# Optimization experiments

Measured on AMD Instinct MI355X. Metric: run time of the kernel, lower is better.

## Reference

```python
import jax, jax.numpy as jnp
import numpy as np

N_LIST = [2048, 2048]
N_CUM = np.cumsum([0] + N_LIST)


def _chamfer(xo, yo):
    # xo: [B, M, 3], yo: [B, N, 3]
    diff = xo[:, :, None, :] - yo[:, None, :, :]        # [B, M, N, 3]
    dist = jnp.sqrt(jnp.sum(diff * diff, axis=-1))       # [B, M, N]
    mean_x = jnp.mean(jnp.min(dist, axis=2))             # x -> nearest y
    mean_y = jnp.mean(jnp.min(dist, axis=1))             # y -> nearest x
    return mean_x + mean_y


def setup_inputs() -> dict:
    key = jax.random.key(0)
    kx, ky = jax.random.split(key)
    x = jax.random.normal(kx, (8, 4096, 3), dtype=jnp.float32)
    y = jax.random.normal(ky, (8, 4096, 3), dtype=jnp.float32)
    return {"x": x, "y": y}


def reference(x, y):
    # loss_type='chamfer', probability=1 -> top-k over ALL distances == plain mean.
    loss = jnp.float32(0.0)
    for i in range(len(N_LIST)):
        lo, hi = int(N_CUM[i]), int(N_CUM[i + 1])
        loss = loss + _chamfer(x[:, lo:hi], y[:, lo:hi])
    return loss
```

## Files before the change

### kernel.cpp

```cpp
#include <hip/hip_runtime.h>
#include <math.h>

typedef float v2f __attribute__((ext_vector_type(2)));

#if __has_builtin(__builtin_elementwise_fma)
#define FMA2(a, b, c) __builtin_elementwise_fma((a), (b), (c))
#else
static __device__ __forceinline__ v2f FMA2(v2f a, v2f b, v2f c) {
    v2f r; r.x = fmaf(a.x, b.x, c.x); r.y = fmaf(a.y, b.y, c.y); return r;
}
#endif

#define NBATCH 8
#define PTOT   4096
#define NG     2048
#define S      16
#define SLEN   (NG / S)
#define QPT    8
#define NT     256
#define NPROB  32
#define NBLK1  (NPROB * S)
#define NPART  (NPROB * S * NG)

__global__ __launch_bounds__(256) void chamfer_pass1(
    const float* __restrict__ x, const float* __restrict__ y,
    float* __restrict__ pmin)
{
    __shared__ float  raw[SLEN * 3];
    __shared__ float4 refX[SLEN / 4];
    __shared__ float4 refY[SLEN / 4];
    __shared__ float4 refZ[SLEN / 4];
    __shared__ float4 refW[SLEN / 4];

    const int blk   = blockIdx.x;
    const int tid   = threadIdx.x;
    const int slice = blk & (S - 1);
    const int prob  = blk >> 4;
    const int dir   = prob >> 4;
    const int bg    = prob & 15;
    const int b     = bg >> 1;
    const int g     = bg & 1;

    const float* qb = (dir == 0 ? x : y) + (size_t)(b * PTOT + g * NG) * 3;
    const float* rb = (dir == 0 ? y : x) + (size_t)(b * PTOT + g * NG) * 3;

    if (tid < (SLEN * 3) / 4) {
        float4 v = ((const float4*)(rb + slice * SLEN * 3))[tid];
        ((float4*)raw)[tid] = v;
    }

    float4 qv[6];
    {
        const float4* qp = (const float4*)(qb + (size_t)tid * QPT * 3);
        #pragma unroll
        for (int i = 0; i < 6; i++) qv[i] = qp[i];
    }

    __syncthreads();

    if (tid < SLEN / 4) {
        const float* p = raw + tid * 12;
        float x0 = p[0], y0 = p[1],  z0 = p[2];
        float x1 = p[3], y1 = p[4],  z1 = p[5];
        float x2 = p[6], y2 = p[7],  z2 = p[8];
        float x3 = p[9], y3 = p[10], z3 = p[11];
        refX[tid] = make_float4(x0, x1, x2, x3);
        refY[tid] = make_float4(y0, y1, y2, y3);
        refZ[tid] = make_float4(z0, z1, z2, z3);
        refW[tid] = make_float4(fmaf(x0, x0, fmaf(y0, y0, z0 * z0)),
                                fmaf(x1, x1, fmaf(y1, y1, z1 * z1)),
                                fmaf(x2, x2, fmaf(y2, y2, z2 * z2)),
                                fmaf(x3, x3, fmaf(y3, y3, z3 * z3)));
    }

    v2f ax2[QPT], ay2[QPT], az2[QPT];
    float qn[QPT], mn[QPT];
    const float* qf = reinterpret_cast<const float*>(qv);
    #pragma unroll
    for (int k = 0; k < QPT; k++) {
        float qx = qf[k * 3 + 0];
        float qy = qf[k * 3 + 1];
        float qz = qf[k * 3 + 2];
        float ax = -2.0f * qx, ay = -2.0f * qy, az = -2.0f * qz;
        ax2[k] = (v2f){ax, ax};
        ay2[k] = (v2f){ay, ay};
        az2[k] = (v2f){az, az};
        qn[k] = fmaf(qx, qx, fmaf(qy, qy, qz * qz));
        mn[k] = 3.4e38f;
    }

    __syncthreads();

    #pragma unroll 2
    for (int n4 = 0; n4 < SLEN / 4; n4++) {
        float4 X = refX[n4], Y = refY[n4], Z = refZ[n4], W = refW[n4];
        v2f X01 = (v2f){X.x, X.y}, X23 = (v2f){X.z, X.w};
        v2f Y01 = (v2f){Y.x, Y.y}, Y23 = (v2f){Y.z, Y.w};
        v2f Z01 = (v2f){Z.x, Z.y}, Z23 = (v2f){Z.z, Z.w};
        v2f W01 = (v2f){W.x, W.y}, W23 = (v2f){W.z, W.w};
        #pragma unroll
        for (int k = 0; k < QPT; k++) {
            v2f t01 = FMA2(X01, ax2[k], W01);
            t01     = FMA2(Y01, ay2[k], t01);
            t01     = FMA2(Z01, az2[k], t01);
            v2f t23 = FMA2(X23, ax2[k], W23);
            t23     = FMA2(Y23, ay2[k], t23);
            t23     = FMA2(Z23, az2[k], t23);
            mn[k] = fminf(fminf(t01.x, t01.y), mn[k]);
            mn[k] = fminf(fminf(t23.x, t23.y), mn[k]);
        }
    }

    float* op = pmin + (size_t)(prob * S + slice) * NG + tid * QPT;
    #pragma unroll
    for (int k = 0; k < QPT; k++)
        op[k] = mn[k] + qn[k];
}

__global__ __launch_bounds__(256) void chamfer_pass2(
    const float* __restrict__ pmin, float* __restrict__ bsum)
{
    __shared__ float s4[4];
    const int gid  = blockIdx.x * 256 + threadIdx.x;
    const int prob = gid >> 11;
    const int q    = gid & (NG - 1);

    float m0 = 3.4e38f, m1 = 3.4e38f;
    #pragma unroll
    for (int s = 0; s < S; s += 2) {
        m0 = fminf(m0, pmin[(size_t)(prob * S + s) * NG + q]);
        m1 = fminf(m1, pmin[(size_t)(prob * S + s + 1) * NG + q]);
    }
    float m = fminf(m0, m1);

    float d = sqrtf(fmaxf(m, 0.0f));

    for (int off = 32; off > 0; off >>= 1)
        d += __shfl_down(d, off, 64);
    if ((threadIdx.x & 63) == 0) s4[threadIdx.x >> 6] = d;
    __syncthreads();
    if (threadIdx.x == 0)
        bsum[blockIdx.x] = (s4[0] + s4[1]) + (s4[2] + s4[3]);
}

__global__ __launch_bounds__(256) void chamfer_pass3(
    const float* __restrict__ bsum, float* __restrict__ out)
{
    __shared__ float s4[4];
    const int tid = threadIdx.x;
    float v = bsum[tid];
    for (int off = 32; off > 0; off >>= 1)
        v += __shfl_down(v, off, 64);
    if ((tid & 63) == 0) s4[tid >> 6] = v;
    __syncthreads();
    if (tid == 0)
        out[0] = ((s4[0] + s4[1]) + (s4[2] + s4[3])) * (1.0f / 16384.0f);
}

extern "C" void kernel_launch(void* const* d_in, const int* in_sizes, int n_in,
                              void* d_out, int out_size, void* d_ws, size_t ws_size,
                              hipStream_t stream) {
    const float* x = (const float*)d_in[0];
    const float* y = (const float*)d_in[1];
    float* out  = (float*)d_out;
    float* pmin = (float*)d_ws;
    float* bsum = pmin + NPART;

    chamfer_pass1<<<NBLK1, NT, 0, stream>>>(x, y, pmin);
    chamfer_pass2<<<256, NT, 0, stream>>>(pmin, bsum);
    chamfer_pass3<<<1, NT, 0, stream>>>(bsum, out);
}
```

Before: 21.83 us.

## Double per-thread query tile and split each block across two reference slices

Each thread now handles 16 queries instead of 8, and each 256-thread block covers two 64-point reference slices, one per half-block. Every shared-memory reference load is therefore reused across more queries, which aims to cut LDS traffic per FMA. The packed FMA is forced through inline v_pk_fma_f32 asm, and the partial minima are written with float4 stores. In exchange, the number of slices doubles, so the partial-min workspace and the data pass2 must read and reduce both double, and register pressure per thread rises.

```diff
diff --git a/kernel.cpp b/kernel.cpp
--- a/kernel.cpp
+++ b/kernel.cpp
@@ -3,39 +3,37 @@
 
 typedef float v2f __attribute__((ext_vector_type(2)));
 
-#if __has_builtin(__builtin_elementwise_fma)
-#define FMA2(a, b, c) __builtin_elementwise_fma((a), (b), (c))
-#else
-static __device__ __forceinline__ v2f FMA2(v2f a, v2f b, v2f c) {
-    v2f r; r.x = fmaf(a.x, b.x, c.x); r.y = fmaf(a.y, b.y, c.y); return r;
+static __device__ __forceinline__ v2f pkfma(v2f a, v2f b, v2f c) {
+    v2f d;
+    asm("v_pk_fma_f32 %0, %1, %2, %3" : "=v"(d) : "v"(a), "v"(b), "v"(c));
+    return d;
 }
-#endif
 
 #define NBATCH 8
 #define PTOT   4096
 #define NG     2048
-#define S      16
+#define S      32
 #define SLEN   (NG / S)
-#define QPT    8
+#define QPT    16
 #define NT     256
 #define NPROB  32
-#define NBLK1  (NPROB * S)
+#define NBLK1  (NPROB * S / 2)
 #define NPART  (NPROB * S * NG)
 
-__global__ __launch_bounds__(256) void chamfer_pass1(
+__global__ __launch_bounds__(256, 2) void chamfer_pass1(
     const float* __restrict__ x, const float* __restrict__ y,
     float* __restrict__ pmin)
 {
-    __shared__ float  raw[SLEN * 3];
-    __shared__ float4 refX[SLEN / 4];
-    __shared__ float4 refY[SLEN / 4];
-    __shared__ float4 refZ[SLEN / 4];
-    __shared__ float4 refW[SLEN / 4];
+    __shared__ float  raw[2 * SLEN * 3];
+    __shared__ float4 refX[2 * SLEN / 4];
+    __shared__ float4 refY[2 * SLEN / 4];
+    __shared__ float4 refZ[2 * SLEN / 4];
+    __shared__ float4 refW[2 * SLEN / 4];
 
     const int blk   = blockIdx.x;
     const int tid   = threadIdx.x;
-    const int slice = blk & (S - 1);
     const int prob  = blk >> 4;
+    const int spair = blk & 15;
     const int dir   = prob >> 4;
     const int bg    = prob & 15;
     const int b     = bg >> 1;
@@ -44,21 +42,23 @@
     const float* qb = (dir == 0 ? x : y) + (size_t)(b * PTOT + g * NG) * 3;
     const float* rb = (dir == 0 ? y : x) + (size_t)(b * PTOT + g * NG) * 3;
 
-    if (tid < (SLEN * 3) / 4) {
-        float4 v = ((const float4*)(rb + slice * SLEN * 3))[tid];
+    if (tid < 96) {
+        float4 v = ((const float4*)(rb + spair * 384))[tid];
         ((float4*)raw)[tid] = v;
     }
 
-    float4 qv[6];
+    const int half = tid >> 7;
+    const int t    = tid & 127;
+    float4 qv[12];
     {
-        const float4* qp = (const float4*)(qb + (size_t)tid * QPT * 3);
+        const float4* qp = (const float4*)qb + (size_t)t * 12;
         #pragma unroll
-        for (int i = 0; i < 6; i++) qv[i] = qp[i];
+        for (int i = 0; i < 12; i++) qv[i] = qp[i];
     }
 
     __syncthreads();
 
-    if (tid < SLEN / 4) {
+    if (tid < 32) {
         const float* p = raw + tid * 12;
         float x0 = p[0], y0 = p[1],  z0 = p[2];
         float x1 = p[3], y1 = p[4],  z1 = p[5];
@@ -73,7 +73,7 @@
                                 fmaf(x3, x3, fmaf(y3, y3, z3 * z3)));
     }
 
-    v2f ax2[QPT], ay2[QPT], az2[QPT];
+    v2f axd[QPT], ayd[QPT], azd[QPT];
     float qn[QPT], mn[QPT];
     const float* qf = reinterpret_cast<const float*>(qv);
     #pragma unroll
@@ -82,17 +82,19 @@
         float qy = qf[k * 3 + 1];
         float qz = qf[k * 3 + 2];
         float ax = -2.0f * qx, ay = -2.0f * qy, az = -2.0f * qz;
-        ax2[k] = (v2f){ax, ax};
-        ay2[k] = (v2f){ay, ay};
-        az2[k] = (v2f){az, az};
+        axd[k] = (v2f){ax, ax};
+        ayd[k] = (v2f){ay, ay};
+        azd[k] = (v2f){az, az};
         qn[k] = fmaf(qx, qx, fmaf(qy, qy, qz * qz));
         mn[k] = 3.4e38f;
     }
 
     __syncthreads();
 
+    const int g0 = half * (SLEN / 4);
     #pragma unroll 2
-    for (int n4 = 0; n4 < SLEN / 4; n4++) {
+    for (int gi = 0; gi < SLEN / 4; gi++) {
+        const int n4 = g0 + gi;
         float4 X = refX[n4], Y = refY[n4], Z = refZ[n4], W = refW[n4];
         v2f X01 = (v2f){X.x, X.y}, X23 = (v2f){X.z, X.w};
         v2f Y01 = (v2f){Y.x, Y.y}, Y23 = (v2f){Y.z, Y.w};
@@ -100,21 +102,26 @@
         v2f W01 = (v2f){W.x, W.y}, W23 = (v2f){W.z, W.w};
         #pragma unroll
         for (int k = 0; k < QPT; k++) {
-            v2f t01 = FMA2(X01, ax2[k], W01);
-            t01     = FMA2(Y01, ay2[k], t01);
-            t01     = FMA2(Z01, az2[k], t01);
-            v2f t23 = FMA2(X23, ax2[k], W23);
-            t23     = FMA2(Y23, ay2[k], t23);
-            t23     = FMA2(Z23, az2[k], t23);
+            v2f t01 = pkfma(X01, axd[k], W01);
+            t01     = pkfma(Y01, ayd[k], t01);
+            t01     = pkfma(Z01, azd[k], t01);
+            v2f t23 = pkfma(X23, axd[k], W23);
+            t23     = pkfma(Y23, ayd[k], t23);
+            t23     = pkfma(Z23, azd[k], t23);
             mn[k] = fminf(fminf(t01.x, t01.y), mn[k]);
             mn[k] = fminf(fminf(t23.x, t23.y), mn[k]);
         }
     }
 
-    float* op = pmin + (size_t)(prob * S + slice) * NG + tid * QPT;
+    const int slice = spair * 2 + half;
+    float* op = pmin + (size_t)(prob * S + slice) * NG + t * QPT;
     #pragma unroll
-    for (int k = 0; k < QPT; k++)
-        op[k] = mn[k] + qn[k];
+    for (int i = 0; i < 4; i++) {
+        ((float4*)op)[i] = make_float4(mn[4*i+0] + qn[4*i+0],
+                                       mn[4*i+1] + qn[4*i+1],
+                                       mn[4*i+2] + qn[4*i+2],
+                                       mn[4*i+3] + qn[4*i+3]);
+    }
 }
 
 __global__ __launch_bounds__(256) void chamfer_pass2(
```

Result: slower. 25.56 us (+17.1%).
